# Optimization experiments

Measured on AMD Instinct MI355X. Metric: run time of the kernel, lower is better.

The kernel has to match this reference:

```python
import jax, jax.numpy as jnp
import numpy as np

B, C, H, W = 4, 64, 64, 64  # x shape; mask is (B,1,8H,8W)


def _conv(x, w, pad=0):
    return jax.lax.conv_general_dilated(
        x, w, (1, 1), [(pad, pad), (pad, pad)],
        dimension_numbers=('NCHW', 'OIHW', 'NCHW'))


def _inorm(x, eps=1e-5):  # InstanceNorm2d, affine=False, biased var (torch default)
    mu = x.mean(axis=(2, 3), keepdims=True)
    var = x.var(axis=(2, 3), keepdims=True)
    return (x - mu) * jax.lax.rsqrt(var + eps)


def _forward(x, mask, kconv_w1, kconv_w2, fs_w1, fs_w2, fs_b2, fs_fuse_w):
    b, c, h, w = x.shape
    n = h * w
    # MaxPool2d(8,8) then binarize
    m = jax.lax.reduce_window(mask, -jnp.inf, jax.lax.max,
                              (1, 1, 8, 8), (1, 1, 8, 8), 'VALID')
    m = (m > 0).astype(x.dtype)
    back = 1.0 - m
    # ResidualBlock K_conv (shared for K and Q paths in original code)
    y = jax.nn.relu(_inorm(_conv(x, kconv_w1, pad=1)))
    y = _inorm(_conv(y, kconv_w2, pad=1))
    kx = jax.nn.relu(y + x)
    # L2-normalized K/Q over channel dim
    K = (kx * back).reshape(b, c, n)
    K = K / (jnp.linalg.norm(K, axis=1, keepdims=True) + 1e-8)
    Q = (kx * m).reshape(b, c, n)
    Q = Q / (jnp.linalg.norm(Q, axis=1, keepdims=True) + 1e-8)
    V = (x * back).reshape(b, c, n)
    # cosine-similarity score map, temperature 20
    score = jnp.einsum('bcq,bck->bqk', Q, K) * 20.0  # (b, n_q, n_k)
    qm = m.reshape(b, 1, n)      # query mask (foreground)
    km = back.reshape(b, 1, n)   # key mask (background)
    NEG = -1000000.0
    validx = score + (1.0 - km) * NEG + (1.0 - qm.transpose(0, 2, 1)) * NEG
    att = jax.nn.softmax(validx, axis=-1) * (qm.transpose(0, 2, 1) * km)
    # att_fore[b,c,q] = sum_k V[b,c,k] * att[b,q,k]
    att_fore = jnp.einsum('bck,bqk->bcq', V, att).reshape(b, c, h, w)
    # Fusion_score
    feat1 = _conv(jnp.concatenate([x * m, att_fore * m], axis=1), fs_w1)
    s = jax.nn.sigmoid(_conv(feat1, fs_w2) + fs_b2[None, :, None, None])
    fused = _conv(jnp.concatenate([x * m, att_fore * m * (1.0 - s)], axis=1), fs_fuse_w)
    fs_out = fused * m + x * (1.0 - m)
    out = fs_out * m + x * (1.0 - m)
    # visualization attention mask
    visatt = att.sum(axis=1).reshape(b, 1, h, w)
    attmask = jnp.repeat(jnp.repeat(visatt, 8, axis=2), 8, axis=3)  # nearest upsample x8
    attmask = attmask / attmask.max()
    return out, attmask


def setup_inputs() -> dict:
    key = jax.random.key(0)
    ks = jax.random.split(key, 8)

    def wgt(k, shape, fan_in):
        return jax.random.normal(k, shape, jnp.float32) / np.sqrt(fan_in)

    x = jax.random.normal(ks[0], (B, C, H, W), jnp.float32)
    # sparse foreground mask so maxpool(8x8)>0 yields a mixed fg/bg mask
    mask = (jax.random.uniform(ks[1], (B, 1, H * 8, W * 8)) < 0.01).astype(jnp.float32)
    return dict(
        x=x, mask=mask,
        kconv_w1=wgt(ks[2], (C, C, 3, 3), C * 9),
        kconv_w2=wgt(ks[3], (C, C, 3, 3), C * 9),
        fs_w1=wgt(ks[4], (C, 2 * C, 1, 1), 2 * C),
        fs_w2=wgt(ks[5], (C, C, 1, 1), C),
        fs_b2=jnp.zeros((C,), jnp.float32),
        fs_fuse_w=wgt(ks[6], (C, 2 * C, 1, 1), 2 * C),
    )


def reference(x, mask, kconv_w1, kconv_w2, fs_w1, fs_w2, fs_b2, fs_fuse_w):
    return _forward(x, mask, kconv_w1, kconv_w2, fs_w1, fs_w2, fs_b2, fs_fuse_w)
```

## Files before the change

### kernel.cpp

```cpp
#include <hip/hip_runtime.h>
#include <hip/hip_bf16.h>

typedef __hip_bfloat16 bf16;
typedef __attribute__((ext_vector_type(8))) short short8;
typedef __attribute__((ext_vector_type(4))) float f32x4;
typedef __attribute__((ext_vector_type(16))) float f32x16;

#define BB 4
#define CC 64
#define NN 4096
#define MH 512
#define MW 512
#define LS 72
#define NPARTS 16
#define NDEN 16

#define WB_AFC  ((size_t)0)
#define WB_VIS  ((size_t)4259840)
#define WB_QIX  ((size_t)4325376)
#define WB_KIX  ((size_t)4390912)
#define WB_MFL  ((size_t)4456448)
#define WB_CNT  ((size_t)4472832)
#define WB_WT1  ((size_t)4476992)
#define WB_WT2  ((size_t)4550720)
#define WB_WFB  ((size_t)4624448)
#define WB_KC   ((size_t)5242880)
#define WB_XT   ((size_t)8388608)
#define WB_KXT  ((size_t)10485760)
#define WB_VT   ((size_t)12582912)
#define WB_QC   ((size_t)14680064)
#define WB_E    ((size_t)16777216)
#define EB_ELEM ((size_t)16777216)
#define WB_AFCP ((size_t)150994944)
#define WB_DENP ((size_t)218103808)
#define WB_VISP ((size_t)220200960)
#define WB_GST  ((size_t)220725248)

__device__ __forceinline__ float us2f(unsigned short u) { return __uint_as_float(((unsigned)u) << 16); }
__device__ __forceinline__ unsigned short f2bu(float f) {
  bf16 h = __float2bfloat16(f);
  return *(unsigned short*)&h;
}

__global__ __launch_bounds__(256) void k_pre(const float* __restrict__ x,
                                             const float* __restrict__ mask,
                                             const float* __restrict__ w1,
                                             const float* __restrict__ w2,
                                             const float* __restrict__ fw1,
                                             const float* __restrict__ fw2,
                                             const float* __restrict__ fwf,
                                             float* __restrict__ outp,
                                             unsigned short* __restrict__ xt,
                                             unsigned char* __restrict__ mfl,
                                             float* __restrict__ vis,
                                             unsigned int* __restrict__ vmaxb,
                                             unsigned short* __restrict__ wT1,
                                             unsigned short* __restrict__ wT2,
                                             unsigned short* __restrict__ wfb) {
  __shared__ float lx[64][65];
  int t = threadIdx.x;
  if (blockIdx.x < 256) {
    int b = blockIdx.x >> 6, p0 = (blockIdx.x & 63) * 64;
    const float* xb = x + (size_t)b * CC * NN + p0;
    float* ob = outp + (size_t)b * CC * NN + p0;
    for (int idx = t; idx < 4096; idx += 256) {
      int c = idx >> 6, j = idx & 63;
      float v = xb[c * NN + j];
      lx[j][c] = v;
      ob[c * NN + j] = v;
    }
    __syncthreads();
    unsigned short* xo = xt + ((size_t)b * NN + p0) * 64;
    for (int idx = t; idx < 2048; idx += 256) {
      int j = idx >> 5, c2 = (idx & 31) * 2;
      ushort2 w2v;
      w2v.x = f2bu(lx[j][c2]);
      w2v.y = f2bu(lx[j][c2 + 1]);
      *(ushort2*)&xo[j * 64 + c2] = w2v;
    }
  } else {
    int g = (blockIdx.x - 256) * 256 + t;
    int o = g >> 2, sub = g & 3;
    int b = o >> 12, p = o & 4095;
    int py = p >> 6, px = p & 63;
    const float* mb = mask + (size_t)b * MH * MW + (py * 8 + sub * 2) * MW + px * 8;
    float mx = 0.f;
    #pragma unroll
    for (int dy = 0; dy < 2; ++dy) {
      const float4* r4 = (const float4*)(mb + dy * MW);
      float4 a = r4[0], c = r4[1];
      mx = fmaxf(mx, fmaxf(fmaxf(a.x, a.y), fmaxf(a.z, a.w)));
      mx = fmaxf(mx, fmaxf(fmaxf(c.x, c.y), fmaxf(c.z, c.w)));
    }
    mx = fmaxf(mx, __shfl_xor(mx, 1));
    mx = fmaxf(mx, __shfl_xor(mx, 2));
    if (sub == 0) {
      mfl[o] = (mx > 0.f) ? 1 : 0;
      vis[o] = 0.f;
    }
    if (g == 0) vmaxb[0] = 0u;
    if (g < 36864) {
      int tap = g >> 12;
      int rem = g & 4095;
      int co = rem >> 6, ci = rem & 63;
      int src = (co * 64 + ci) * 9 + tap;
      wT1[g] = f2bu(w1[src]);
      wT2[g] = f2bu(w2[src]);
    } else if (g < 57344) {
      int j2 = g - 36864;
      if (j2 < 8192)       wfb[j2] = f2bu(fw1[j2]);
      else if (j2 < 12288) wfb[j2] = f2bu(fw2[j2 - 8192]);
      else                 wfb[j2] = f2bu(fwf[j2 - 12288]);
    }
  }
}

__global__ __launch_bounds__(256) void k_compact(const unsigned char* __restrict__ mfl,
                                                 int* __restrict__ qidx, int* __restrict__ kidx,
                                                 int* __restrict__ nq, int* __restrict__ nk) {
  int b = blockIdx.x;
  __shared__ unsigned char lm[4096];
  int t = threadIdx.x;
  *(uint4*)&lm[t * 16] = *(const uint4*)&mfl[b * NN + t * 16];
  __syncthreads();
  if (t >= 64) return;
  int lane = t;
  int qb = 0, kb = 0;
  #pragma unroll
  for (int it = 0; it < 64; ++it) {
    int p = it * 64 + lane;
    bool f = lm[p] != 0;
    unsigned long long bal = __ballot(f);
    int before = __popcll(bal & ((1ULL << lane) - 1ULL));
    if (f)  qidx[b * NN + qb + before] = p;
    if (!f) kidx[b * NN + kb + (lane - before)] = p;
    int cnt = __popcll(bal);
    qb += cnt; kb += 64 - cnt;
  }
  if (lane == 0) { nq[b] = qb; nk[b] = kb; }
}

template <bool NORM_IN>
__global__ __launch_bounds__(256) void k_convm(const unsigned short* __restrict__ src,
                                               const unsigned short* __restrict__ wT,
                                               const float* __restrict__ insum,
                                               const float* __restrict__ insq,
                                               unsigned short* __restrict__ dst,
                                               float* __restrict__ gsump,
                                               float* __restrict__ gsqp) {
  int b = blockIdx.y;
  int r = blockIdx.x;
  __shared__ unsigned short bx[198 * LS];
  __shared__ float nmean[64], ninv[64];
  int t = threadIdx.x;
  if (NORM_IN) {
    if (t < 64) {
      float s = 0.f, s2v = 0.f;
      #pragma unroll 8
      for (int r2 = 0; r2 < 64; ++r2) {
        s   += insum[((size_t)r2 * BB + b) * 64 + t];
        s2v += insq [((size_t)r2 * BB + b) * 64 + t];
      }
      float m = s * (1.f / NN);
      float v = fmaxf(s2v * (1.f / NN) - m * m, 0.f);
      nmean[t] = m; ninv[t] = rsqrtf(v + 1e-5f);
    }
    __syncthreads();
  }
  const unsigned short* sb = src + (size_t)b * NN * 64;
  for (int idx = t; idx < 198 * 8; idx += 256) {
    int row = idx >> 3, c8 = (idx & 7) * 8;
    int dy = row / 66;
    int cx = row - dy * 66 - 1;
    int rr = r + dy - 1;
    uint4 v = make_uint4(0u, 0u, 0u, 0u);
    if ((unsigned)rr < 64u && (unsigned)cx < 64u) {
      v = *(const uint4*)(sb + ((size_t)(rr * 64 + cx)) * 64 + c8);
      if (NORM_IN) {
        unsigned short* e = (unsigned short*)&v;
        #pragma unroll
        for (int j = 0; j < 8; ++j)
          e[j] = f2bu(fmaxf((us2f(e[j]) - nmean[c8 + j]) * ninv[c8 + j], 0.f));
      }
    }
    *(uint4*)&bx[row * LS + c8] = v;
  }
  __syncthreads();
  int lane = t & 63;
  int quad = lane >> 4, col = lane & 15;
  int qw = (t >> 6) * 16;
  f32x4 acc[4] = {{0.f,0.f,0.f,0.f},{0.f,0.f,0.f,0.f},{0.f,0.f,0.f,0.f},{0.f,0.f,0.f,0.f}};
  #pragma unroll
  for (int tap = 0; tap < 9; ++tap) {
    int dy = tap / 3, dx = tap - dy * 3 - 1;
    const unsigned short* wrow = wT + ((size_t)tap * 64 + qw + col) * 64;
    short8 a0 = *(const short8*)(wrow + quad * 8);
    short8 a1 = *(const short8*)(wrow + 32 + quad * 8);
    int rbase = dy * 66 + dx + 1;
    #pragma unroll
    for (int nt = 0; nt < 4; ++nt) {
      int row = rbase + nt * 16 + col;
      short8 b0 = *(const short8*)&bx[row * LS + quad * 8];
      short8 b1 = *(const short8*)&bx[row * LS + 32 + quad * 8];
      acc[nt] = __builtin_amdgcn_mfma_f32_16x16x32_bf16(a0, b0, acc[nt], 0, 0, 0);
      acc[nt] = __builtin_amdgcn_mfma_f32_16x16x32_bf16(a1, b1, acc[nt], 0, 0, 0);
    }
  }
  #pragma unroll
  for (int rr = 0; rr < 4; ++rr) {
    float s1 = acc[0][rr] + acc[1][rr] + acc[2][rr] + acc[3][rr];
    float s2 = acc[0][rr]*acc[0][rr] + acc[1][rr]*acc[1][rr]
             + acc[2][rr]*acc[2][rr] + acc[3][rr]*acc[3][rr];
    s1 += __shfl_xor(s1, 1); s2 += __shfl_xor(s2, 1);
    s1 += __shfl_xor(s1, 2); s2 += __shfl_xor(s2, 2);
    s1 += __shfl_xor(s1, 4); s2 += __shfl_xor(s2, 4);
    s1 += __shfl_xor(s1, 8); s2 += __shfl_xor(s2, 8);
    if (col == 0) {
      int co = qw + quad * 4 + rr;
      gsump[((size_t)r * BB + b) * 64 + co] = s1;
      gsqp [((size_t)r * BB + b) * 64 + co] = s2;
    }
  }
  __syncthreads();
  #pragma unroll
  for (int nt = 0; nt < 4; ++nt)
    #pragma unroll
    for (int rr = 0; rr < 4; ++rr)
      bx[(nt * 16 + col) * LS + qw + quad * 4 + rr] = f2bu(acc[nt][rr]);
  __syncthreads();
  unsigned short* db = dst + ((size_t)b * NN + r * 64) * 64;
  for (int idx = t; idx < 512; idx += 256) {
    int px = idx >> 3, c8 = (idx & 7) * 8;
    *(uint4*)(db + (size_t)px * 64 + c8) = *(const uint4*)&bx[px * LS + c8];
  }
}

__global__ __launch_bounds__(256) void k_knorm(unsigned short* __restrict__ kxt,
                                               const unsigned short* __restrict__ xt,
                                               const float* __restrict__ gsump,
                                               const float* __restrict__ gsqp) {
  int b = blockIdx.x >> 6;
  int p0 = (blockIdx.x & 63) * 64;
  __shared__ float m2[64], i2[64];
  int t = threadIdx.x;
  if (t < 64) {
    float s = 0.f, s2v = 0.f;
    #pragma unroll 8
    for (int r2 = 0; r2 < 64; ++r2) {
      s   += gsump[((size_t)r2 * BB + b) * 64 + t];
      s2v += gsqp [((size_t)r2 * BB + b) * 64 + t];
    }
    float m = s * (1.f / NN);
    float v = fmaxf(s2v * (1.f / NN) - m * m, 0.f);
    m2[t] = m; i2[t] = rsqrtf(v + 1e-5f);
  }
  __syncthreads();
  int px = t >> 2, c0 = (t & 3) * 16;
  size_t base = ((size_t)b * NN + p0 + px) * 64 + c0;
  unsigned short kv[16], xv[16];
  *(uint4*)&kv[0] = *(const uint4*)(kxt + base);
  *(uint4*)&kv[8] = *(const uint4*)(kxt + base + 8);
  *(uint4*)&xv[0] = *(const uint4*)(xt + base);
  *(uint4*)&xv[8] = *(const uint4*)(xt + base + 8);
  float v[16]; float ss = 0.f;
  #pragma unroll
  for (int j = 0; j < 16; ++j) {
    float f = fmaxf((us2f(kv[j]) - m2[c0 + j]) * i2[c0 + j] + us2f(xv[j]), 0.f);
    v[j] = f; ss += f * f;
  }
  ss += __shfl_xor(ss, 1);
  ss += __shfl_xor(ss, 2);
  float inv = 1.f / (sqrtf(ss) + 1e-8f);
  #pragma unroll
  for (int j = 0; j < 16; ++j) kv[j] = f2bu(v[j] * inv);
  *(uint4*)(kxt + base) = *(const uint4*)&kv[0];
  *(uint4*)(kxt + base + 8) = *(const uint4*)&kv[8];
}

__global__ __launch_bounds__(256) void k_gath(const unsigned short* __restrict__ khat,
                                              const unsigned short* __restrict__ xt,
                                              const int* __restrict__ qidx, const int* __restrict__ kidx,
                                              const int* __restrict__ nqv, const int* __restrict__ nkv,
                                              unsigned short* __restrict__ kc,
                                              unsigned short* __restrict__ vt,
                                              unsigned short* __restrict__ qc) {
  int b = blockIdx.y;
  int j0 = blockIdx.x * 64;
  int nqb = nqv[b], nkb = nkv[b];
  int NKP = (nkb + 63) & ~63, NQP = (nqb + 63) & ~63;
  bool dok = j0 < NKP, doq = j0 < NQP;
  if (!dok && !doq) return;
  __shared__ int li[128];
  __shared__ unsigned short tv[64 * LS];
  int t = threadIdx.x;
  if (t < 64) li[t] = (j0 + t < nkb) ? kidx[b * NN + j0 + t] : -1;
  if (t >= 64 && t < 128) li[t] = (j0 + (t - 64) < nqb) ? qidx[b * NN + j0 + (t - 64)] : -1;
  __syncthreads();
  const unsigned short* khb = khat + (size_t)b * NN * 64;
  const unsigned short* xtb = xt + (size_t)b * NN * 64;
  uint4 z = make_uint4(0u, 0u, 0u, 0u);
  for (int idx = t; idx < 512; idx += 256) {
    int row = idx >> 3, c8 = (idx & 7) * 8;
    size_t dsto = ((size_t)b * NN + j0 + row) * 64 + c8;
    if (dok) {
      int sk = li[row];
      *(uint4*)(kc + dsto) = (sk >= 0) ? *(const uint4*)(khb + (size_t)sk * 64 + c8) : z;
      *(uint4*)&tv[row * LS + c8] = (sk >= 0) ? *(const uint4*)(xtb + (size_t)sk * 64 + c8) : z;
    }
    if (doq) {
      int sq = li[64 + row];
      *(uint4*)(qc + dsto) = (sq >= 0) ? *(const uint4*)(khb + (size_t)sq * 64 + c8) : z;
    }
  }
  __syncthreads();
  if (!dok) return;
  for (int idx = t; idx < 512; idx += 256) {
    int c = idx >> 3, k8 = (idx & 7) * 8;
    unsigned short vals[8];
    #pragma unroll
    for (int j = 0; j < 8; ++j) vals[j] = tv[(k8 + j) * LS + c];
    *(uint4*)(vt + (size_t)b * 262144 + (size_t)c * 4096 + j0 + k8) = *(const uint4*)&vals[0];
  }
}

__global__ __launch_bounds__(256) void k_att1(const unsigned short* __restrict__ kc,
                                              const unsigned short* __restrict__ vt,
                                              const unsigned short* __restrict__ qc,
                                              const int* __restrict__ nqv, const int* __restrict__ nkv,
                                              unsigned short* __restrict__ afc_part,
                                              float* __restrict__ den_part,
                                              unsigned short* __restrict__ eg) {
  __shared__ unsigned short leb[4][32 * LS];
  int b = blockIdx.y;
  int nqb = nqv[b], nkb = nkv[b];
  int t = threadIdx.x;
  int wave = t >> 6, lane = t & 63;
  int part = blockIdx.x & (NPARTS - 1);
  int q0 = ((blockIdx.x >> 4) * 4 + wave) * 32;
  if (q0 >= nqb) return;
  int ntiles = (nkb + 63) >> 6;
  int nt_blk = (part < ntiles) ? ((ntiles - part + NPARTS - 1) >> 4) : 0;
  int NKP = (nkb + 63) & ~63;
  unsigned short* le = leb[wave];
  int l31 = lane & 31, lhi = lane >> 5;
  const unsigned short* kcb = kc + (size_t)b * NN * 64;
  const unsigned short* vtb = vt + (size_t)b * 262144;
  const unsigned short* qcb = qc + (size_t)b * NN * 64;
  unsigned short* egb = eg + (size_t)b * EB_ELEM;
  unsigned short* afcp = afc_part + (((size_t)part * BB + b) * NN) * 64;
  float* denp = den_part + ((size_t)part * BB + b) * NN;
  short8 aq[4];
  #pragma unroll
  for (int ks = 0; ks < 4; ++ks)
    aq[ks] = *(const short8*)(qcb + (size_t)(q0 + l31) * 64 + ks * 16 + lhi * 8);
  f32x16 pv0, pv1, dsum;
  #pragma unroll
  for (int i = 0; i < 16; ++i) { pv0[i] = 0.f; pv1[i] = 0.f; dsum[i] = 0.f; }
  for (int it = 0; it < nt_blk; ++it) {
    int j0 = (part + it * NPARTS) * 64;
    #pragma unroll
    for (int kh = 0; kh < 2; ++kh) {
      f32x16 s;
      #pragma unroll
      for (int i = 0; i < 16; ++i) s[i] = 0.f;
      const unsigned short* krow = kcb + (size_t)(j0 + kh * 32 + l31) * 64 + lhi * 8;
      #pragma unroll
      for (int ks = 0; ks < 4; ++ks) {
        short8 bk = *(const short8*)(krow + ks * 16);
        s = __builtin_amdgcn_mfma_f32_32x32x16_bf16(aq[ks], bk, s, 0, 0, 0);
      }
      bool kval = (j0 + kh * 32 + l31) < nkb;
      #pragma unroll
      for (int reg = 0; reg < 16; ++reg) {
        float e = kval ? __expf(20.f * s[reg]) : 0.f;
        dsum[reg] += e;
        int row = (reg & 3) + 8 * (reg >> 2) + 4 * lhi;
        le[row * LS + kh * 32 + l31] = f2bu(e);
      }
    }
    #pragma unroll
    for (int ks = 0; ks < 4; ++ks) {
      short8 a = *(const short8*)&le[l31 * LS + ks * 16 + lhi * 8];
      short8 bv0 = *(const short8*)(vtb + (size_t)l31 * 4096 + j0 + ks * 16 + lhi * 8);
      short8 bv1 = *(const short8*)(vtb + (size_t)(32 + l31) * 4096 + j0 + ks * 16 + lhi * 8);
      pv0 = __builtin_amdgcn_mfma_f32_32x32x16_bf16(a, bv0, pv0, 0, 0, 0);
      pv1 = __builtin_amdgcn_mfma_f32_32x32x16_bf16(a, bv1, pv1, 0, 0, 0);
    }
    #pragma unroll
    for (int sub = 0; sub < 4; ++sub) {
      int idx = sub * 64 + lane;
      int q = idx >> 3, cc8 = (idx & 7) * 8;
      if (q0 + q < nqb)
        *(uint4*)(egb + (size_t)(q0 + q) * NKP + j0 + cc8) = *(const uint4*)&le[q * LS + cc8];
    }
  }
  #pragma unroll
  for (int reg = 0; reg < 16; ++reg) {
    float v = dsum[reg];
    v += __shfl_xor(v, 1); v += __shfl_xor(v, 2); v += __shfl_xor(v, 4);
    v += __shfl_xor(v, 8); v += __shfl_xor(v, 16);
    int row = (reg & 3) + 8 * (reg >> 2) + 4 * lhi;
    int qq = q0 + row;
    if (l31 == 0 && qq < nqb) denp[qq] = v;
  }
  #pragma unroll
  for (int reg = 0; reg < 16; ++reg) {
    int row = (reg & 3) + 8 * (reg >> 2) + 4 * lhi;
    int qq = q0 + row;
    if (qq < nqb) {
      afcp[(size_t)qq * 64 + l31]      = f2bu(pv0[reg]);
      afcp[(size_t)qq * 64 + 32 + l31] = f2bu(pv1[reg]);
    }
  }
}

__global__ __launch_bounds__(256) void k_vis(const unsigned short* __restrict__ eg,
                                             const float* __restrict__ den_part,
                                             const int* __restrict__ nqv, const int* __restrict__ nkv,
                                             float* __restrict__ visp) {
  int b = blockIdx.z;
  int nqb = nqv[b], nkb = nkv[b];
  int k0 = blockIdx.x * 256;
  if (k0 >= nkb) return;
  int NKP = (nkb + 63) & ~63;
  int qpart = blockIdx.y;
  int qbeg = (qpart * nqb) >> 3;
  int qend = ((qpart + 1) * nqb) >> 3;
  __shared__ float wd[256];
  int t = threadIdx.x;
  int k = k0 + t;
  const unsigned short* eb = eg + (size_t)b * EB_ELEM;
  float acc = 0.f;
  for (int qc = qbeg; qc < qend; qc += 256) {
    __syncthreads();
    int qq = qc + t;
    float d = 0.f;
    if (qq < qend) {
      #pragma unroll
      for (int p2 = 0; p2 < NDEN; ++p2) d += den_part[((size_t)p2 * BB + b) * NN + qq];
    }
    wd[t] = (d > 0.f) ? 1.f / d : 0.f;
    __syncthreads();
    int lim = min(256, qend - qc);
    if (k < nkb) {
      const unsigned short* ep = eb + (size_t)qc * NKP + k;
      int j = 0;
      for (; j + 8 <= lim; j += 8) {
        #pragma unroll
        for (int u = 0; u < 8; ++u)
          acc += us2f(ep[(size_t)(j + u) * NKP]) * wd[j + u];
      }
      for (; j < lim; ++j)
        acc += us2f(ep[(size_t)j * NKP]) * wd[j];
    }
  }
  if (k < nkb) visp[((size_t)qpart * BB + b) * NN + k] = acc;
}

#define FS 136
__global__ __launch_bounds__(256) void k_fusionm(const unsigned short* __restrict__ xt,
                                                 const unsigned short* __restrict__ afc_part,
                                                 const float* __restrict__ den_part,
                                                 const int* __restrict__ qidx, const int* __restrict__ nqv,
                                                 const unsigned short* __restrict__ wall,
                                                 const float* __restrict__ b2,
                                                 float* __restrict__ outp) {
  int b = blockIdx.y;
  int nqb = nqv[b];
  int q0 = blockIdx.x * 64;
  if (q0 >= nqb) return;
  __shared__ unsigned short pxa[64 * FS];
  __shared__ unsigned short f1s[64 * LS];
  __shared__ int qpl[64];
  int t = threadIdx.x;
  int lane = t & 63;
  int quad = lane >> 4, col = lane & 15;
  int cb = (t >> 6) * 16;
  const int* qix = qidx + b * NN;
  const unsigned short* xtb = xt + (size_t)b * NN * 64;
  const unsigned short* w1b = wall;
  const unsigned short* w2b = wall + 8192;
  const unsigned short* wfb = wall + 12288;
  short8 a1[4], a2[2], af[4];
  #pragma unroll
  for (int kt = 0; kt < 4; ++kt) {
    a1[kt] = *(const short8*)&w1b[(cb + col) * 128 + kt * 32 + quad * 8];
    af[kt] = *(const short8*)&wfb[(cb + col) * 128 + kt * 32 + quad * 8];
  }
  #pragma unroll
  for (int kt = 0; kt < 2; ++kt)
    a2[kt] = *(const short8*)&w2b[(cb + col) * 64 + kt * 32 + quad * 8];
  float b2v[4];
  #pragma unroll
  for (int r = 0; r < 4; ++r) b2v[r] = b2[cb + quad * 4 + r];
  if (t < 64) qpl[t] = (q0 + t < nqb) ? qix[q0 + t] : -1;
  for (int idx = t; idx < 512; idx += 256) {
    int q = idx >> 3, c8 = (idx & 7) * 8;
    int qq = q0 + q;
    uint4 pv = make_uint4(0u, 0u, 0u, 0u);
    unsigned short pa8[8] = {0, 0, 0, 0, 0, 0, 0, 0};
    if (qq < nqb) {
      int qp = qix[qq];
      pv = *(const uint4*)(xtb + (size_t)qp * 64 + c8);
      float d = 0.f;
      #pragma unroll
      for (int p2 = 0; p2 < NDEN; ++p2)
        d += den_part[((size_t)p2 * BB + b) * NN + qq];
      float av[8];
      #pragma unroll
      for (int j = 0; j < 8; ++j) av[j] = 0.f;
      #pragma unroll
      for (int p2 = 0; p2 < NPARTS; ++p2) {
        const uint4 u = *(const uint4*)(afc_part + (((size_t)p2 * BB + b) * NN + qq) * 64 + c8);
        const unsigned short* e8 = (const unsigned short*)&u;
        #pragma unroll
        for (int j = 0; j < 8; ++j) av[j] += us2f(e8[j]);
      }
      float invd = (d > 0.f) ? 1.f / d : 0.f;
      #pragma unroll
      for (int j = 0; j < 8; ++j) pa8[j] = f2bu(av[j] * invd);
    }
    *(uint4*)&pxa[q * FS + c8] = pv;
    *(uint4*)&pxa[q * FS + 64 + c8] = *(const uint4*)&pa8[0];
  }
  __syncthreads();
  #pragma unroll
  for (int qt = 0; qt < 4; ++qt) {
    f32x4 acc = {0.f, 0.f, 0.f, 0.f};
    #pragma unroll
    for (int kt = 0; kt < 4; ++kt) {
      short8 bfrag = *(const short8*)&pxa[(qt * 16 + col) * FS + kt * 32 + quad * 8];
      acc = __builtin_amdgcn_mfma_f32_16x16x32_bf16(a1[kt], bfrag, acc, 0, 0, 0);
    }
    #pragma unroll
    for (int r = 0; r < 4; ++r)
      f1s[(qt * 16 + col) * LS + cb + quad * 4 + r] = f2bu(acc[r]);
  }
  __syncthreads();
  #pragma unroll
  for (int qt = 0; qt < 4; ++qt) {
    f32x4 acc = {0.f, 0.f, 0.f, 0.f};
    #pragma unroll
    for (int kt = 0; kt < 2; ++kt) {
      short8 bfrag = *(const short8*)&f1s[(qt * 16 + col) * LS + kt * 32 + quad * 8];
      acc = __builtin_amdgcn_mfma_f32_16x16x32_bf16(a2[kt], bfrag, acc, 0, 0, 0);
    }
    #pragma unroll
    for (int r = 0; r < 4; ++r) {
      float sg = 1.f / (1.f + __expf(-(acc[r] + b2v[r])));
      int addr = (qt * 16 + col) * FS + 64 + cb + quad * 4 + r;
      pxa[addr] = f2bu(us2f(pxa[addr]) * (1.f - sg));
    }
  }
  __syncthreads();
  #pragma unroll
  for (int qt = 0; qt < 4; ++qt) {
    f32x4 acc = {0.f, 0.f, 0.f, 0.f};
    #pragma unroll
    for (int kt = 0; kt < 4; ++kt) {
      short8 bfrag = *(const short8*)&pxa[(qt * 16 + col) * FS + kt * 32 + quad * 8];
      acc = __builtin_amdgcn_mfma_f32_16x16x32_bf16(af[kt], bfrag, acc, 0, 0, 0);
    }
    int qp = qpl[qt * 16 + col];
    if (qp >= 0) {
      #pragma unroll
      for (int r = 0; r < 4; ++r)
        outp[((size_t)b * CC + cb + quad * 4 + r) * NN + qp] = acc[r];
    }
  }
}

__global__ __launch_bounds__(256) void k_vmax(const float* __restrict__ visp,
                                              const int* __restrict__ kidx,
                                              const int* __restrict__ nkv,
                                              float* __restrict__ vis,
                                              unsigned int* __restrict__ vmaxb) {
  int i = blockIdx.x * 256 + threadIdx.x;
  int b = i >> 12, k = i & 4095;
  float v = 0.f;
  if (k < nkv[b]) {
    #pragma unroll
    for (int p2 = 0; p2 < 8; ++p2) v += visp[((size_t)p2 * BB + b) * NN + k];
    vis[b * NN + kidx[b * NN + k]] = v;
  }
  #pragma unroll
  for (int off = 32; off > 0; off >>= 1) v = fmaxf(v, __shfl_down(v, off));
  if ((threadIdx.x & 63) == 0) atomicMax(vmaxb, __float_as_uint(v));
}

__global__ __launch_bounds__(256) void k_upsample(const float* __restrict__ vis,
                                                  const unsigned int* __restrict__ vmaxb,
                                                  float* __restrict__ out2) {
  int i4 = blockIdx.x * 256 + threadIdx.x;
  int b = i4 >> 16;
  int rem = i4 & 65535;
  int y = rem >> 7, x4 = (rem & 127) * 4;
  float vm = __uint_as_float(vmaxb[0]);
  if (!(vm > 0.f)) vm = 1.f;
  float v = vis[b * NN + (y >> 3) * 64 + (x4 >> 3)] / vm;
  ((float4*)out2)[i4] = make_float4(v, v, v, v);
}

extern "C" void kernel_launch(void* const* d_in, const int* in_sizes, int n_in,
                              void* d_out, int out_size, void* d_ws, size_t ws_size,
                              hipStream_t stream) {
  const float* x    = (const float*)d_in[0];
  const float* mask = (const float*)d_in[1];
  const float* w1   = (const float*)d_in[2];
  const float* w2c  = (const float*)d_in[3];
  const float* fsw1 = (const float*)d_in[4];
  const float* fsw2 = (const float*)d_in[5];
  const float* fsb2 = (const float*)d_in[6];
  const float* fswf = (const float*)d_in[7];
  float* out = (float*)d_out;
  char* wsb = (char*)d_ws;

  float* vis = (float*)(wsb + WB_VIS);
  int* qidx  = (int*)(wsb + WB_QIX);
  int* kidx  = (int*)(wsb + WB_KIX);
  unsigned char* mfl = (unsigned char*)(wsb + WB_MFL);
  int* nq = (int*)(wsb + WB_CNT);
  int* nk = nq + 4;
  unsigned int* vmaxb = (unsigned int*)(nq + 8);
  unsigned short* wT1 = (unsigned short*)(wsb + WB_WT1);
  unsigned short* wT2 = (unsigned short*)(wsb + WB_WT2);
  unsigned short* wall = (unsigned short*)(wsb + WB_WFB);
  unsigned short* y1t = (unsigned short*)(wsb + WB_AFC);
  unsigned short* xt  = (unsigned short*)(wsb + WB_XT);
  unsigned short* kxt = (unsigned short*)(wsb + WB_KXT);
  unsigned short* khat = kxt;
  unsigned short* kc  = (unsigned short*)(wsb + WB_KC);
  unsigned short* vt  = (unsigned short*)(wsb + WB_VT);
  unsigned short* qc  = (unsigned short*)(wsb + WB_QC);
  unsigned short* eg  = (unsigned short*)(wsb + WB_E);
  unsigned short* afc_part = (unsigned short*)(wsb + WB_AFCP);
  float* den_part = (float*)(wsb + WB_DENP);
  float* visp     = (float*)(wsb + WB_VISP);
  float* gsum1p = (float*)(wsb + WB_GST);
  float* gsq1p  = (float*)(wsb + WB_GST + 65536);
  float* gsum2p = (float*)(wsb + WB_GST + 131072);
  float* gsq2p  = (float*)(wsb + WB_GST + 196608);

  k_pre<<<512, 256, 0, stream>>>(x, mask, w1, w2c, fsw1, fsw2, fswf,
                                 out, xt, mfl, vis, vmaxb, wT1, wT2, wall);
  k_compact<<<4, 256, 0, stream>>>(mfl, qidx, kidx, nq, nk);
  k_convm<false><<<dim3(64, BB), 256, 0, stream>>>(xt, wT1, nullptr, nullptr, y1t, gsum1p, gsq1p);
  k_convm<true><<<dim3(64, BB), 256, 0, stream>>>(y1t, wT2, gsum1p, gsq1p, kxt, gsum2p, gsq2p);
  k_knorm<<<256, 256, 0, stream>>>(kxt, xt, gsum2p, gsq2p);
  k_gath<<<dim3(64, BB), 256, 0, stream>>>(khat, xt, qidx, kidx, nq, nk, kc, vt, qc);
  k_att1<<<dim3(32 * NPARTS, BB), 256, 0, stream>>>(kc, vt, qc, nq, nk, afc_part, den_part, eg);
  k_vis<<<dim3(16, 8, BB), 256, 0, stream>>>(eg, den_part, nq, nk, visp);
  k_fusionm<<<dim3(64, BB), 256, 0, stream>>>(xt, afc_part, den_part, qidx, nq, wall, fsb2, out);
  k_vmax<<<64, 256, 0, stream>>>(visp, kidx, nk, vis, vmaxb);
  k_upsample<<<1024, 256, 0, stream>>>(vis, vmaxb, out + 1048576);
}
```

Before: 176.2 us.

## Write fused output compactly then scatter via inverse index in a new kernel

```diff
diff --git a/kernel.cpp b/kernel.cpp
--- a/kernel.cpp
+++ b/kernel.cpp
@@ -15,7 +15,7 @@
 #define NPARTS 16
 #define NDEN 16
 
-#define WB_AFC  ((size_t)0)
+#define WB_FOUT ((size_t)0)
 #define WB_VIS  ((size_t)4259840)
 #define WB_QIX  ((size_t)4325376)
 #define WB_KIX  ((size_t)4390912)
@@ -35,6 +35,7 @@
 #define WB_DENP ((size_t)218103808)
 #define WB_VISP ((size_t)220200960)
 #define WB_GST  ((size_t)220725248)
+#define WB_QNV  ((size_t)220987392)
 
 __device__ __forceinline__ float us2f(unsigned short u) { return __uint_as_float(((unsigned)u) << 16); }
 __device__ __forceinline__ unsigned short f2bu(float f) {
@@ -49,7 +50,6 @@
                                              const float* __restrict__ fw1,
                                              const float* __restrict__ fw2,
                                              const float* __restrict__ fwf,
-                                             float* __restrict__ outp,
                                              unsigned short* __restrict__ xt,
                                              unsigned char* __restrict__ mfl,
                                              float* __restrict__ vis,
@@ -62,12 +62,9 @@
   if (blockIdx.x < 256) {
     int b = blockIdx.x >> 6, p0 = (blockIdx.x & 63) * 64;
     const float* xb = x + (size_t)b * CC * NN + p0;
-    float* ob = outp + (size_t)b * CC * NN + p0;
     for (int idx = t; idx < 4096; idx += 256) {
       int c = idx >> 6, j = idx & 63;
-      float v = xb[c * NN + j];
-      lx[j][c] = v;
-      ob[c * NN + j] = v;
+      lx[j][c] = xb[c * NN + j];
     }
     __syncthreads();
     unsigned short* xo = xt + ((size_t)b * NN + p0) * 64;
@@ -117,6 +114,7 @@
 
 __global__ __launch_bounds__(256) void k_compact(const unsigned char* __restrict__ mfl,
                                                  int* __restrict__ qidx, int* __restrict__ kidx,
+                                                 int* __restrict__ qinv,
                                                  int* __restrict__ nq, int* __restrict__ nk) {
   int b = blockIdx.x;
   __shared__ unsigned char lm[4096];
@@ -132,8 +130,8 @@
     bool f = lm[p] != 0;
     unsigned long long bal = __ballot(f);
     int before = __popcll(bal & ((1ULL << lane) - 1ULL));
-    if (f)  qidx[b * NN + qb + before] = p;
-    if (!f) kidx[b * NN + kb + (lane - before)] = p;
+    if (f)  { qidx[b * NN + qb + before] = p; qinv[b * NN + p] = qb + before; }
+    else    { kidx[b * NN + kb + (lane - before)] = p; qinv[b * NN + p] = -1; }
     int cnt = __popcll(bal);
     qb += cnt; kb += 64 - cnt;
   }
@@ -347,8 +345,8 @@
   const unsigned short* vtb = vt + (size_t)b * 262144;
   const unsigned short* qcb = qc + (size_t)b * NN * 64;
   unsigned short* egb = eg + (size_t)b * EB_ELEM;
-  unsigned short* afcp = afc_part + (((size_t)part * BB + b) * NN) * 64;
-  float* denp = den_part + ((size_t)part * BB + b) * NN;
+  unsigned short* afcp = afc_part + ((size_t)b * NN) * (NPARTS * 64);
+  float* denp = den_part + ((size_t)b * NN) * NDEN;
   short8 aq[4];
   #pragma unroll
   for (int ks = 0; ks < 4; ++ks)
@@ -401,15 +399,16 @@
     v += __shfl_xor(v, 8); v += __shfl_xor(v, 16);
     int row = (reg & 3) + 8 * (reg >> 2) + 4 * lhi;
     int qq = q0 + row;
-    if (l31 == 0 && qq < nqb) denp[qq] = v;
+    if (l31 == 0 && qq < nqb) denp[(size_t)qq * NDEN + part] = v;
   }
   #pragma unroll
   for (int reg = 0; reg < 16; ++reg) {
     int row = (reg & 3) + 8 * (reg >> 2) + 4 * lhi;
     int qq = q0 + row;
     if (qq < nqb) {
-      afcp[(size_t)qq * 64 + l31]      = f2bu(pv0[reg]);
-      afcp[(size_t)qq * 64 + 32 + l31] = f2bu(pv1[reg]);
+      unsigned short* ap = afcp + ((size_t)qq * NPARTS + part) * 64;
+      ap[l31]      = f2bu(pv0[reg]);
+      ap[32 + l31] = f2bu(pv1[reg]);
     }
   }
 }
@@ -436,8 +435,10 @@
     int qq = qc + t;
     float d = 0.f;
     if (qq < qend) {
-      #pragma unroll
-      for (int p2 = 0; p2 < NDEN; ++p2) d += den_part[((size_t)p2 * BB + b) * NN + qq];
+      const float4* dp = (const float4*)(den_part + ((size_t)b * NN + qq) * NDEN);
+      float4 a0 = dp[0], a1 = dp[1], a2 = dp[2], a3 = dp[3];
+      d = ((a0.x + a0.y) + (a0.z + a0.w)) + ((a1.x + a1.y) + (a1.z + a1.w))
+        + ((a2.x + a2.y) + (a2.z + a2.w)) + ((a3.x + a3.y) + (a3.z + a3.w));
     }
     wd[t] = (d > 0.f) ? 1.f / d : 0.f;
     __syncthreads();
@@ -464,14 +465,13 @@
                                                  const int* __restrict__ qidx, const int* __restrict__ nqv,
                                                  const unsigned short* __restrict__ wall,
                                                  const float* __restrict__ b2,
-                                                 float* __restrict__ outp) {
+                                                 float* __restrict__ fout) {
   int b = blockIdx.y;
   int nqb = nqv[b];
   int q0 = blockIdx.x * 64;
   if (q0 >= nqb) return;
   __shared__ unsigned short pxa[64 * FS];
   __shared__ unsigned short f1s[64 * LS];
-  __shared__ int qpl[64];
   int t = threadIdx.x;
   int lane = t & 63;
   int quad = lane >> 4, col = lane & 15;
@@ -493,7 +493,6 @@
   float b2v[4];
   #pragma unroll
   for (int r = 0; r < 4; ++r) b2v[r] = b2[cb + quad * 4 + r];
-  if (t < 64) qpl[t] = (q0 + t < nqb) ? qix[q0 + t] : -1;
   for (int idx = t; idx < 512; idx += 256) {
     int q = idx >> 3, c8 = (idx & 7) * 8;
     int qq = q0 + q;
@@ -502,16 +501,17 @@
     if (qq < nqb) {
       int qp = qix[qq];
       pv = *(const uint4*)(xtb + (size_t)qp * 64 + c8);
+      const float* db = den_part + ((size_t)b * NN + qq) * NDEN;
       float d = 0.f;
       #pragma unroll
-      for (int p2 = 0; p2 < NDEN; ++p2)
-        d += den_part[((size_t)p2 * BB + b) * NN + qq];
+      for (int p2 = 0; p2 < NDEN; ++p2) d += db[p2];
       float av[8];
       #pragma unroll
       for (int j = 0; j < 8; ++j) av[j] = 0.f;
+      const unsigned short* ab = afc_part + ((size_t)b * NN + qq) * (NPARTS * 64) + c8;
       #pragma unroll
       for (int p2 = 0; p2 < NPARTS; ++p2) {
-        const uint4 u = *(const uint4*)(afc_part + (((size_t)p2 * BB + b) * NN + qq) * 64 + c8);
+        const uint4 u = *(const uint4*)(ab + p2 * 64);
         const unsigned short* e8 = (const unsigned short*)&u;
         #pragma unroll
         for (int j = 0; j < 8; ++j) av[j] += us2f(e8[j]);
@@ -561,12 +561,49 @@
       short8 bfrag = *(const short8*)&pxa[(qt * 16 + col) * FS + kt * 32 + quad * 8];
       acc = __builtin_amdgcn_mfma_f32_16x16x32_bf16(af[kt], bfrag, acc, 0, 0, 0);
     }
-    int qp = qpl[qt * 16 + col];
-    if (qp >= 0) {
-      #pragma unroll
-      for (int r = 0; r < 4; ++r)
-        outp[((size_t)b * CC + cb + quad * 4 + r) * NN + qp] = acc[r];
-    }
+    int qq = q0 + qt * 16 + col;
+    if (qq < nqb) {
+      float* fo = fout + ((size_t)b * NN + qq) * 64 + cb + quad * 4;
+      *(float4*)fo = make_float4(acc[0], acc[1], acc[2], acc[3]);
+    }
+  }
+}
+
+__global__ __launch_bounds__(256) void k_scat(const float* __restrict__ x,
+                                              const float* __restrict__ fout,
+                                              const int* __restrict__ qinv,
+                                              float* __restrict__ outp) {
+  int b = blockIdx.y, p0 = blockIdx.x * 64;
+  __shared__ float lt[64][65];
+  __shared__ int lq[64];
+  int t = threadIdx.x;
+  if (t < 64) lq[t] = qinv[b * NN + p0 + t];
+  const float* xb = x + (size_t)b * CC * NN;
+  for (int idx = t; idx < 512; idx += 256) {
+    int c = idx >> 3, j8 = (idx & 7) * 8;
+    const float4* s4 = (const float4*)(xb + (size_t)c * NN + p0 + j8);
+    float4 a = s4[0], v = s4[1];
+    lt[c][j8 + 0] = a.x; lt[c][j8 + 1] = a.y; lt[c][j8 + 2] = a.z; lt[c][j8 + 3] = a.w;
+    lt[c][j8 + 4] = v.x; lt[c][j8 + 5] = v.y; lt[c][j8 + 6] = v.z; lt[c][j8 + 7] = v.w;
+  }
+  __syncthreads();
+  for (int idx = t; idx < 512; idx += 256) {
+    int j = idx >> 3, c0 = (idx & 7) * 8;
+    int q = lq[j];
+    if (q >= 0) {
+      const float4* f4 = (const float4*)(fout + ((size_t)b * NN + q) * 64 + c0);
+      float4 a = f4[0], v = f4[1];
+      lt[c0 + 0][j] = a.x; lt[c0 + 1][j] = a.y; lt[c0 + 2][j] = a.z; lt[c0 + 3][j] = a.w;
+      lt[c0 + 4][j] = v.x; lt[c0 + 5][j] = v.y; lt[c0 + 6][j] = v.z; lt[c0 + 7][j] = v.w;
+    }
+  }
+  __syncthreads();
+  float* ob = outp + (size_t)b * CC * NN;
+  for (int idx = t; idx < 512; idx += 256) {
+    int c = idx >> 3, j8 = (idx & 7) * 8;
+    float4* d4 = (float4*)(ob + (size_t)c * NN + p0 + j8);
+    d4[0] = make_float4(lt[c][j8 + 0], lt[c][j8 + 1], lt[c][j8 + 2], lt[c][j8 + 3]);
+    d4[1] = make_float4(lt[c][j8 + 4], lt[c][j8 + 5], lt[c][j8 + 6], lt[c][j8 + 7]);
   }
 }
 
@@ -618,6 +655,7 @@
   float* vis = (float*)(wsb + WB_VIS);
   int* qidx  = (int*)(wsb + WB_QIX);
   int* kidx  = (int*)(wsb + WB_KIX);
+  int* qinv  = (int*)(wsb + WB_QNV);
   unsigned char* mfl = (unsigned char*)(wsb + WB_MFL);
   int* nq = (int*)(wsb + WB_CNT);
   int* nk = nq + 4;
@@ -625,7 +663,8 @@
   unsigned short* wT1 = (unsigned short*)(wsb + WB_WT1);
   unsigned short* wT2 = (unsigned short*)(wsb + WB_WT2);
   unsigned short* wall = (unsigned short*)(wsb + WB_WFB);
-  unsigned short* y1t = (unsigned short*)(wsb + WB_AFC);
+  unsigned short* y1t = (unsigned short*)(wsb + WB_FOUT);
+  float* fout = (float*)(wsb + WB_FOUT);
   unsigned short* xt  = (unsigned short*)(wsb + WB_XT);
   unsigned short* kxt = (unsigned short*)(wsb + WB_KXT);
   unsigned short* khat = kxt;
@@ -642,15 +681,16 @@
   float* gsq2p  = (float*)(wsb + WB_GST + 196608);
 
   k_pre<<<512, 256, 0, stream>>>(x, mask, w1, w2c, fsw1, fsw2, fswf,
-                                 out, xt, mfl, vis, vmaxb, wT1, wT2, wall);
-  k_compact<<<4, 256, 0, stream>>>(mfl, qidx, kidx, nq, nk);
+                                 xt, mfl, vis, vmaxb, wT1, wT2, wall);
+  k_compact<<<4, 256, 0, stream>>>(mfl, qidx, kidx, qinv, nq, nk);
   k_convm<false><<<dim3(64, BB), 256, 0, stream>>>(xt, wT1, nullptr, nullptr, y1t, gsum1p, gsq1p);
   k_convm<true><<<dim3(64, BB), 256, 0, stream>>>(y1t, wT2, gsum1p, gsq1p, kxt, gsum2p, gsq2p);
   k_knorm<<<256, 256, 0, stream>>>(kxt, xt, gsum2p, gsq2p);
   k_gath<<<dim3(64, BB), 256, 0, stream>>>(khat, xt, qidx, kidx, nq, nk, kc, vt, qc);
   k_att1<<<dim3(32 * NPARTS, BB), 256, 0, stream>>>(kc, vt, qc, nq, nk, afc_part, den_part, eg);
   k_vis<<<dim3(16, 8, BB), 256, 0, stream>>>(eg, den_part, nq, nk, visp);
-  k_fusionm<<<dim3(64, BB), 256, 0, stream>>>(xt, afc_part, den_part, qidx, nq, wall, fsb2, out);
+  k_fusionm<<<dim3(64, BB), 256, 0, stream>>>(xt, afc_part, den_part, qidx, nq, wall, fsb2, fout);
+  k_scat<<<dim3(64, BB), 256, 0, stream>>>(x, fout, qinv, out);
   k_vmax<<<64, 256, 0, stream>>>(visp, kidx, nk, vis, vmaxb);
   k_upsample<<<1024, 256, 0, stream>>>(vis, vmaxb, out + 1048576);
 }
```

Measured after the change: 181.5 us. +3.0%, slower.

## Fuse instance-norm/residual/L2-normalize into gather kernel and transpose partial-sum layout

Applied to the files above, without the earlier changes.

```diff
diff --git a/kernel.cpp b/kernel.cpp
--- a/kernel.cpp
+++ b/kernel.cpp
@@ -15,7 +15,7 @@
 #define NPARTS 16
 #define NDEN 16
 
-#define WB_AFC  ((size_t)0)
+#define WB_Y1T  ((size_t)0)
 #define WB_VIS  ((size_t)4259840)
 #define WB_QIX  ((size_t)4325376)
 #define WB_KIX  ((size_t)4390912)
@@ -235,52 +235,12 @@
   }
 }
 
-__global__ __launch_bounds__(256) void k_knorm(unsigned short* __restrict__ kxt,
-                                               const unsigned short* __restrict__ xt,
-                                               const float* __restrict__ gsump,
-                                               const float* __restrict__ gsqp) {
-  int b = blockIdx.x >> 6;
-  int p0 = (blockIdx.x & 63) * 64;
-  __shared__ float m2[64], i2[64];
-  int t = threadIdx.x;
-  if (t < 64) {
-    float s = 0.f, s2v = 0.f;
-    #pragma unroll 8
-    for (int r2 = 0; r2 < 64; ++r2) {
-      s   += gsump[((size_t)r2 * BB + b) * 64 + t];
-      s2v += gsqp [((size_t)r2 * BB + b) * 64 + t];
-    }
-    float m = s * (1.f / NN);
-    float v = fmaxf(s2v * (1.f / NN) - m * m, 0.f);
-    m2[t] = m; i2[t] = rsqrtf(v + 1e-5f);
-  }
-  __syncthreads();
-  int px = t >> 2, c0 = (t & 3) * 16;
-  size_t base = ((size_t)b * NN + p0 + px) * 64 + c0;
-  unsigned short kv[16], xv[16];
-  *(uint4*)&kv[0] = *(const uint4*)(kxt + base);
-  *(uint4*)&kv[8] = *(const uint4*)(kxt + base + 8);
-  *(uint4*)&xv[0] = *(const uint4*)(xt + base);
-  *(uint4*)&xv[8] = *(const uint4*)(xt + base + 8);
-  float v[16]; float ss = 0.f;
-  #pragma unroll
-  for (int j = 0; j < 16; ++j) {
-    float f = fmaxf((us2f(kv[j]) - m2[c0 + j]) * i2[c0 + j] + us2f(xv[j]), 0.f);
-    v[j] = f; ss += f * f;
-  }
-  ss += __shfl_xor(ss, 1);
-  ss += __shfl_xor(ss, 2);
-  float inv = 1.f / (sqrtf(ss) + 1e-8f);
-  #pragma unroll
-  for (int j = 0; j < 16; ++j) kv[j] = f2bu(v[j] * inv);
-  *(uint4*)(kxt + base) = *(const uint4*)&kv[0];
-  *(uint4*)(kxt + base + 8) = *(const uint4*)&kv[8];
-}
-
-__global__ __launch_bounds__(256) void k_gath(const unsigned short* __restrict__ khat,
+__global__ __launch_bounds__(256) void k_gath(const unsigned short* __restrict__ kxt,
                                               const unsigned short* __restrict__ xt,
                                               const int* __restrict__ qidx, const int* __restrict__ kidx,
                                               const int* __restrict__ nqv, const int* __restrict__ nkv,
+                                              const float* __restrict__ gsump,
+                                              const float* __restrict__ gsqp,
                                               unsigned short* __restrict__ kc,
                                               unsigned short* __restrict__ vt,
                                               unsigned short* __restrict__ qc) {
@@ -292,11 +252,24 @@
   if (!dok && !doq) return;
   __shared__ int li[128];
   __shared__ unsigned short tv[64 * LS];
+  __shared__ float m2[64], i2[64];
   int t = threadIdx.x;
   if (t < 64) li[t] = (j0 + t < nkb) ? kidx[b * NN + j0 + t] : -1;
   if (t >= 64 && t < 128) li[t] = (j0 + (t - 64) < nqb) ? qidx[b * NN + j0 + (t - 64)] : -1;
-  __syncthreads();
-  const unsigned short* khb = khat + (size_t)b * NN * 64;
+  if (t >= 128 && t < 192) {
+    int c = t - 128;
+    float s = 0.f, s2v = 0.f;
+    #pragma unroll 8
+    for (int r2 = 0; r2 < 64; ++r2) {
+      s   += gsump[((size_t)r2 * BB + b) * 64 + c];
+      s2v += gsqp [((size_t)r2 * BB + b) * 64 + c];
+    }
+    float m = s * (1.f / NN);
+    float v = fmaxf(s2v * (1.f / NN) - m * m, 0.f);
+    m2[c] = m; i2[c] = rsqrtf(v + 1e-5f);
+  }
+  __syncthreads();
+  const unsigned short* kxb = kxt + (size_t)b * NN * 64;
   const unsigned short* xtb = xt + (size_t)b * NN * 64;
   uint4 z = make_uint4(0u, 0u, 0u, 0u);
   for (int idx = t; idx < 512; idx += 256) {
@@ -304,12 +277,55 @@
     size_t dsto = ((size_t)b * NN + j0 + row) * 64 + c8;
     if (dok) {
       int sk = li[row];
-      *(uint4*)(kc + dsto) = (sk >= 0) ? *(const uint4*)(khb + (size_t)sk * 64 + c8) : z;
-      *(uint4*)&tv[row * LS + c8] = (sk >= 0) ? *(const uint4*)(xtb + (size_t)sk * 64 + c8) : z;
+      uint4 ko = z;
+      if (sk >= 0) {
+        uint4 kv = *(const uint4*)(kxb + (size_t)sk * 64 + c8);
+        uint4 xv = *(const uint4*)(xtb + (size_t)sk * 64 + c8);
+        const unsigned short* ke = (const unsigned short*)&kv;
+        const unsigned short* xe = (const unsigned short*)&xv;
+        float f[8]; float ss = 0.f;
+        #pragma unroll
+        for (int j = 0; j < 8; ++j) {
+          float v = fmaxf((us2f(ke[j]) - m2[c8 + j]) * i2[c8 + j] + us2f(xe[j]), 0.f);
+          f[j] = v; ss += v * v;
+        }
+        ss += __shfl_xor(ss, 1); ss += __shfl_xor(ss, 2); ss += __shfl_xor(ss, 4);
+        float inv = 1.f / (sqrtf(ss) + 1e-8f);
+        unsigned short* oe = (unsigned short*)&ko;
+        #pragma unroll
+        for (int j = 0; j < 8; ++j) oe[j] = f2bu(f[j] * inv);
+        *(uint4*)&tv[row * LS + c8] = xv;
+      } else {
+        float ss = 0.f;
+        ss += __shfl_xor(ss, 1); ss += __shfl_xor(ss, 2); ss += __shfl_xor(ss, 4);
+        *(uint4*)&tv[row * LS + c8] = z;
+      }
+      *(uint4*)(kc + dsto) = ko;
     }
     if (doq) {
       int sq = li[64 + row];
-      *(uint4*)(qc + dsto) = (sq >= 0) ? *(const uint4*)(khb + (size_t)sq * 64 + c8) : z;
+      uint4 qo = z;
+      if (sq >= 0) {
+        uint4 kv = *(const uint4*)(kxb + (size_t)sq * 64 + c8);
+        uint4 xv = *(const uint4*)(xtb + (size_t)sq * 64 + c8);
+        const unsigned short* ke = (const unsigned short*)&kv;
+        const unsigned short* xe = (const unsigned short*)&xv;
+        float f[8]; float ss = 0.f;
+        #pragma unroll
+        for (int j = 0; j < 8; ++j) {
+          float v = fmaxf((us2f(ke[j]) - m2[c8 + j]) * i2[c8 + j] + us2f(xe[j]), 0.f);
+          f[j] = v; ss += v * v;
+        }
+        ss += __shfl_xor(ss, 1); ss += __shfl_xor(ss, 2); ss += __shfl_xor(ss, 4);
+        float inv = 1.f / (sqrtf(ss) + 1e-8f);
+        unsigned short* oe = (unsigned short*)&qo;
+        #pragma unroll
+        for (int j = 0; j < 8; ++j) oe[j] = f2bu(f[j] * inv);
+      } else {
+        float ss = 0.f;
+        ss += __shfl_xor(ss, 1); ss += __shfl_xor(ss, 2); ss += __shfl_xor(ss, 4);
+      }
+      *(uint4*)(qc + dsto) = qo;
     }
   }
   __syncthreads();
@@ -347,8 +363,8 @@
   const unsigned short* vtb = vt + (size_t)b * 262144;
   const unsigned short* qcb = qc + (size_t)b * NN * 64;
   unsigned short* egb = eg + (size_t)b * EB_ELEM;
-  unsigned short* afcp = afc_part + (((size_t)part * BB + b) * NN) * 64;
-  float* denp = den_part + ((size_t)part * BB + b) * NN;
+  unsigned short* afcp = afc_part + ((size_t)b * NN) * (NPARTS * 64);
+  float* denp = den_part + ((size_t)b * NN) * NDEN;
   short8 aq[4];
   #pragma unroll
   for (int ks = 0; ks < 4; ++ks)
@@ -401,15 +417,16 @@
     v += __shfl_xor(v, 8); v += __shfl_xor(v, 16);
     int row = (reg & 3) + 8 * (reg >> 2) + 4 * lhi;
     int qq = q0 + row;
-    if (l31 == 0 && qq < nqb) denp[qq] = v;
+    if (l31 == 0 && qq < nqb) denp[(size_t)qq * NDEN + part] = v;
   }
   #pragma unroll
   for (int reg = 0; reg < 16; ++reg) {
     int row = (reg & 3) + 8 * (reg >> 2) + 4 * lhi;
     int qq = q0 + row;
     if (qq < nqb) {
-      afcp[(size_t)qq * 64 + l31]      = f2bu(pv0[reg]);
-      afcp[(size_t)qq * 64 + 32 + l31] = f2bu(pv1[reg]);
+      unsigned short* ap = afcp + ((size_t)qq * NPARTS + part) * 64;
+      ap[l31]      = f2bu(pv0[reg]);
+      ap[32 + l31] = f2bu(pv1[reg]);
     }
   }
 }
@@ -436,8 +453,10 @@
     int qq = qc + t;
     float d = 0.f;
     if (qq < qend) {
-      #pragma unroll
-      for (int p2 = 0; p2 < NDEN; ++p2) d += den_part[((size_t)p2 * BB + b) * NN + qq];
+      const float4* dp = (const float4*)(den_part + ((size_t)b * NN + qq) * NDEN);
+      float4 a0 = dp[0], a1 = dp[1], a2 = dp[2], a3 = dp[3];
+      d = ((a0.x + a0.y) + (a0.z + a0.w)) + ((a1.x + a1.y) + (a1.z + a1.w))
+        + ((a2.x + a2.y) + (a2.z + a2.w)) + ((a3.x + a3.y) + (a3.z + a3.w));
     }
     wd[t] = (d > 0.f) ? 1.f / d : 0.f;
     __syncthreads();
@@ -502,16 +521,17 @@
     if (qq < nqb) {
       int qp = qix[qq];
       pv = *(const uint4*)(xtb + (size_t)qp * 64 + c8);
+      const float* db = den_part + ((size_t)b * NN + qq) * NDEN;
       float d = 0.f;
       #pragma unroll
-      for (int p2 = 0; p2 < NDEN; ++p2)
-        d += den_part[((size_t)p2 * BB + b) * NN + qq];
+      for (int p2 = 0; p2 < NDEN; ++p2) d += db[p2];
       float av[8];
       #pragma unroll
       for (int j = 0; j < 8; ++j) av[j] = 0.f;
+      const unsigned short* ab = afc_part + ((size_t)b * NN + qq) * (NPARTS * 64) + c8;
       #pragma unroll
       for (int p2 = 0; p2 < NPARTS; ++p2) {
-        const uint4 u = *(const uint4*)(afc_part + (((size_t)p2 * BB + b) * NN + qq) * 64 + c8);
+        const uint4 u = *(const uint4*)(ab + p2 * 64);
         const unsigned short* e8 = (const unsigned short*)&u;
         #pragma unroll
         for (int j = 0; j < 8; ++j) av[j] += us2f(e8[j]);
@@ -625,10 +645,9 @@
   unsigned short* wT1 = (unsigned short*)(wsb + WB_WT1);
   unsigned short* wT2 = (unsigned short*)(wsb + WB_WT2);
   unsigned short* wall = (unsigned short*)(wsb + WB_WFB);
-  unsigned short* y1t = (unsigned short*)(wsb + WB_AFC);
+  unsigned short* y1t = (unsigned short*)(wsb + WB_Y1T);
   unsigned short* xt  = (unsigned short*)(wsb + WB_XT);
   unsigned short* kxt = (unsigned short*)(wsb + WB_KXT);
-  unsigned short* khat = kxt;
   unsigned short* kc  = (unsigned short*)(wsb + WB_KC);
   unsigned short* vt  = (unsigned short*)(wsb + WB_VT);
   unsigned short* qc  = (unsigned short*)(wsb + WB_QC);
@@ -646,8 +665,7 @@
   k_compact<<<4, 256, 0, stream>>>(mfl, qidx, kidx, nq, nk);
   k_convm<false><<<dim3(64, BB), 256, 0, stream>>>(xt, wT1, nullptr, nullptr, y1t, gsum1p, gsq1p);
   k_convm<true><<<dim3(64, BB), 256, 0, stream>>>(y1t, wT2, gsum1p, gsq1p, kxt, gsum2p, gsq2p);
-  k_knorm<<<256, 256, 0, stream>>>(kxt, xt, gsum2p, gsq2p);
-  k_gath<<<dim3(64, BB), 256, 0, stream>>>(khat, xt, qidx, kidx, nq, nk, kc, vt, qc);
+  k_gath<<<dim3(64, BB), 256, 0, stream>>>(kxt, xt, qidx, kidx, nq, nk, gsum2p, gsq2p, kc, vt, qc);
   k_att1<<<dim3(32 * NPARTS, BB), 256, 0, stream>>>(kc, vt, qc, nq, nk, afc_part, den_part, eg);
   k_vis<<<dim3(16, 8, BB), 256, 0, stream>>>(eg, den_part, nq, nk, visp);
   k_fusionm<<<dim3(64, BB), 256, 0, stream>>>(xt, afc_part, den_part, qidx, nq, wall, fsb2, out);
```

Measured after the change: 174.0 us. No clear change (-1.3%).
